# Kernel optimization log

Hardware: AMD Instinct MI355X
Metric: run time of the kernel (lower is better)

Reference implementation:

```python
import jax, jax.numpy as jnp
import numpy as np

B, N, F_IN, HID, HEADS, LAYERS = 512, 128, 128, 64, 4, 3
NEG_SLOPE = 0.2  # DenseGATConv default


def setup_inputs() -> dict:
    key = jax.random.key(0)
    ks = jax.random.split(key, 1 + 4 * LAYERS)
    inp = {}
    inp["x"] = jax.random.normal(ks[0], (B * N, F_IN), jnp.float32)
    # uniform graph sizes: graph i owns nodes [i*N, (i+1)*N)
    inp["batch_mask"] = jnp.repeat(jnp.arange(B, dtype=jnp.int32), N)
    dims = [F_IN] + [HID * HEADS] * (LAYERS - 1)
    for l in range(LAYERS):
        d = dims[l]
        k = 4 * l
        inp[f"W{l}"] = jax.random.normal(ks[1 + k], (d, HEADS * HID), jnp.float32) / np.sqrt(d)
        inp[f"att_src{l}"] = jax.random.normal(ks[2 + k], (HEADS, HID), jnp.float32) * 0.1
        inp[f"att_dst{l}"] = jax.random.normal(ks[3 + k], (HEADS, HID), jnp.float32) * 0.1
        inp[f"b{l}"] = jnp.zeros((HEADS * HID,), jnp.float32)  # zero-init bias, as in PyG
    return inp


def _dense_gat(x, adj, W, att_src, att_dst, bias):
    # x: [B, N, F_in], adj: [N, N] (shared structure, broadcast over batch)
    b, n, _ = x.shape
    h = (x @ W).reshape(b, n, HEADS, HID)                       # [B,N,H,C]
    a_src = jnp.einsum('bnhc,hc->bnh', h, att_src)              # [B,N,H]
    a_dst = jnp.einsum('bnhc,hc->bnh', h, att_dst)              # [B,N,H]
    # alpha[b,i,j,h] = a_src[b,j,h] + a_dst[b,i,h]
    alpha = a_src[:, None, :, :] + a_dst[:, :, None, :]         # [B,N,N,H]
    alpha = jnp.where(alpha >= 0, alpha, NEG_SLOPE * alpha)
    alpha = jnp.where(adj[None, :, :, None] == 0, -jnp.inf, alpha)
    alpha = jax.nn.softmax(alpha, axis=2)                       # softmax over sources j
    out = jnp.einsum('bijh,bjhc->bihc', alpha, h)               # [B,N,H,C]
    return out.reshape(b, n, HEADS * HID) + bias                # concat heads + bias


def reference(x, batch_mask, W0, att_src0, att_dst0, b0,
              W1, att_src1, att_dst1, b1, W2, att_src2, att_dst2, b2):
    # to_dense_batch with uniform graph sizes == reshape; batch_mask encodes this layout
    h = x.reshape(B, N, F_IN)
    eye = jnp.eye(N, dtype=x.dtype)
    # GNNBlock builds full adjacency with zeroed diagonal ...
    adj = jnp.ones((N, N), x.dtype) - eye
    # ... and DenseGATConv(add_loop=True) re-adds self-loops
    adj = jnp.maximum(adj, eye)
    params = [(W0, att_src0, att_dst0, b0), (W1, att_src1, att_dst1, b1),
              (W2, att_src2, att_dst2, b2)]
    for (W, a_s, a_d, b) in params:
        h = _dense_gat(h, adj, W, a_s, a_d, b)
        # block act is nn.LeakyReLU(True): negative_slope=True==1.0 -> identity
        h = jnp.where(h >= 0, h, 1.0 * h)
    return h.sum(axis=1)  # [B, HEADS*HID]
```

## Files before the change

kernel.cpp:

```cpp
#include <hip/hip_runtime.h>
#include <hip/hip_bf16.h>


typedef unsigned short u16;
typedef __attribute__((ext_vector_type(8))) short short8;
typedef __attribute__((ext_vector_type(4))) float f32x4;

#define L2E 1.44269504088896340736f

__device__ __forceinline__ u16 f2bf(float f) {
  unsigned int u = __float_as_uint(f);
  u += 0x7fffu + ((u >> 16) & 1u);
  return (u16)(u >> 16);
}
__device__ __forceinline__ unsigned int pk2(float a, float b) {
  __hip_bfloat162 h2 = __float22bfloat162_rn(make_float2(a, b));
  unsigned int u;
  __builtin_memcpy(&u, &h2, 4);
  return u;
}

__device__ __forceinline__ int xs_byte(int row, int col) {
  return (row << 9) + ((col << 1) ^ ((row & 7) << 4));
}
__device__ __forceinline__ int ht_byte(int row, int col) {
  return (row << 8) + ((col << 1) ^ ((row & 7) << 4));
}

__global__ void prep_w(const float* __restrict__ W0, const float* __restrict__ W1,
                       const float* __restrict__ W2,
                       const float* __restrict__ as0, const float* __restrict__ ad0,
                       const float* __restrict__ as1, const float* __restrict__ ad1,
                       const float* __restrict__ as2, const float* __restrict__ ad2,
                       u16* __restrict__ wt) {
  const int bid = blockIdx.x, tid = threadIdx.x;
  if (bid < 80) {
    const float* W; int NKB, base, rel;
    if (bid < 16)      { W = W0; NKB = 4; base = 0;      rel = bid; }
    else if (bid < 48) { W = W1; NKB = 8; base = 34816;  rel = bid - 16; }
    else               { W = W2; NKB = 8; base = 104448; rel = bid - 48; }
    const int kb = rel >> 2, ko = rel & 3;
    const int n = tid;
    union { u16 v[8]; short8 s; } u;
    #pragma unroll
    for (int e = 0; e < 8; ++e)
      u.v[e] = f2bf(W[(kb * 32 + ko * 8 + e) * 256 + n]);
    const int t = n >> 4, l15 = n & 15;
    *(short8*)(wt + base + (((t * NKB + kb) * 64 + l15 + (ko << 4)) << 3)) = u.s;
  } else if (bid < 100) {
    int b2 = bid - 80;
    const float* W; const float* as; const float* ad; int NKB, base, kb;
    if (b2 < 4)       { W = W0; as = as0; ad = ad0; NKB = 4; base = 0;      kb = b2; }
    else if (b2 < 12) { W = W1; as = as1; ad = ad1; NKB = 8; base = 34816;  kb = b2 - 4; }
    else              { W = W2; as = as2; ad = ad2; NKB = 8; base = 104448; kb = b2 - 12; }
    const int kloc = tid >> 3, col = tid & 7, h = col & 3;
    const int k = kb * 32 + kloc;
    const float* av = (col < 4) ? as : ad;
    float acc = 0.f;
    #pragma unroll 8
    for (int c = 0; c < 64; ++c)
      acc = fmaf(W[k * 256 + h * 64 + c], av[h * 64 + c], acc);
    const int lane2 = col + ((kloc >> 3) << 4), e = kloc & 7;
    const int tb = base + ((16 * NKB + kb) << 9);
    wt[tb + ((lane2) << 3) + e]     = f2bf(acc);
    wt[tb + ((lane2 + 8) << 3) + e] = 0;
  }
}

__global__ __launch_bounds__(1024, 4) void gat_all(
    const float* __restrict__ x, const u16* __restrict__ wt,
    const float* __restrict__ bb0, const float* __restrict__ bb1,
    const float* __restrict__ bb2, float* __restrict__ out)
{
  constexpr int AB = 0;
  constexpr int SB = 65536;
  constexpr int DB = 67584;
  constexpr int PM = 69632;
  constexpr int BS = 69696;
  constexpr int OA = 70720;
  __shared__ __align__(16) unsigned char smem[71744];

  float* sbuf  = (float*)(smem + SB);
  float* dbuf  = (float*)(smem + DB);
  float* pmaxw = (float*)(smem + PM);
  float* bsb   = (float*)(smem + BS);
  float* oac   = (float*)(smem + OA);

  const int b    = blockIdx.x;
  const int tid  = threadIdx.x;
  const int w    = tid >> 6;
  const int lane = tid & 63;
  const int l15  = lane & 15;
  const int lg   = lane >> 4;

  {
    const float4* xg = (const float4*)(x + (size_t)b * (128 * 128));
    #pragma unroll
    for (int it = 0; it < 4; ++it) {
      int e = tid + it * 1024;
      float4 v = xg[e];
      int row = e >> 5, c = (e & 31) << 2;
      uint2 u = { pk2(v.x, v.y), pk2(v.z, v.w) };
      *(uint2*)(smem + AB + xs_byte(row, c)) = u;
    }
  }
  __syncthreads();

  const u16* wfl[3]    = {wt, wt + 34816, wt + 104448};
  const float* bias[3] = {bb0, bb1, bb2};

  #pragma unroll
  for (int l = 0; l < 3; ++l) {
    const int NKB = (l == 0) ? 4 : 8;
    const u16* wf = wfl[l];

    if (tid < 256) {
      bsb[tid] = bias[l][tid];
      if (l == 2) oac[tid] = 0.f;
    }

    const int mw = w & 1, nw = w >> 1;
    f32x4 acc[4][2] = {};
    for (int ks = 0; ks < NKB; ++ks) {
      const int kcol = ks * 32 + lg * 8;
      short8 afr[4];
      #pragma unroll
      for (int mi = 0; mi < 4; ++mi)
        afr[mi] = *(const short8*)(smem + AB + xs_byte(mw * 64 + mi * 16 + l15, kcol));
      short8 bfr[2];
      #pragma unroll
      for (int ni = 0; ni < 2; ++ni) {
        int t = nw * 2 + ni;
        bfr[ni] = *(const short8*)(wf + (((t * NKB + ks) * 64 + lane) << 3));
      }
      #pragma unroll
      for (int mi = 0; mi < 4; ++mi)
        #pragma unroll
        for (int ni = 0; ni < 2; ++ni)
          acc[mi][ni] = __builtin_amdgcn_mfma_f32_16x16x32_bf16(
              afr[mi], bfr[ni], acc[mi][ni], 0, 0, 0);
    }

    if (w >= 12) {
      const int mw2 = w & 1, mih = (w >> 1) & 1;
      f32x4 acc2[2] = {};
      for (int ks = 0; ks < NKB; ++ks) {
        const int kcol = ks * 32 + lg * 8;
        short8 bsd = *(const short8*)(wf + (((16 * NKB + ks) * 64 + lane) << 3));
        #pragma unroll
        for (int mi2 = 0; mi2 < 2; ++mi2) {
          short8 a = *(const short8*)(smem + AB +
              xs_byte(mw2 * 64 + (mih * 2 + mi2) * 16 + l15, kcol));
          acc2[mi2] = __builtin_amdgcn_mfma_f32_16x16x32_bf16(a, bsd, acc2[mi2], 0, 0, 0);
        }
      }
      float mx = -3.4e38f;
      #pragma unroll
      for (int mi2 = 0; mi2 < 2; ++mi2) {
        f32x4 v = acc2[mi2] * L2E;
        if (l15 < 8) {
          float* basep = (float*)(smem + (l15 < 4 ? SB : DB))
                       + (l15 & 3) * 128 + mw2 * 64 + (mih * 2 + mi2) * 16 + lg * 4;
          *(float4*)basep = (float4){v[0], v[1], v[2], v[3]};
        }
        mx = fmaxf(mx, fmaxf(fmaxf(v[0], v[1]), fmaxf(v[2], v[3])));
      }
      mx = fmaxf(mx, __shfl_xor(mx, 16));
      mx = fmaxf(mx, __shfl_xor(mx, 32));
      if (lane < 4) pmaxw[lane * 4 + (w - 12)] = mx;
    }
    __syncthreads();

    #pragma unroll
    for (int mi = 0; mi < 4; ++mi) {
      int j0 = mw * 64 + mi * 16 + lg * 4;
      #pragma unroll
      for (int ni = 0; ni < 2; ++ni) {
        int c = nw * 32 + ni * 16 + l15;
        uint2 u = { pk2(acc[mi][ni][0], acc[mi][ni][1]),
                    pk2(acc[mi][ni][2], acc[mi][ni][3]) };
        *(uint2*)(smem + AB + ht_byte(c, j0)) = u;
      }
    }
    __syncthreads();

    {
      const int hw = w >> 2, q = w & 3;
      f32x4 facc[4][2] = {};
      float den[2] = {0.f, 0.f};
      float dvv[2], nml[2];
      const float smax = fmaxf(fmaxf(pmaxw[hw * 4], pmaxw[hw * 4 + 1]),
                               fmaxf(pmaxw[hw * 4 + 2], pmaxw[hw * 4 + 3]));
      #pragma unroll
      for (int ni = 0; ni < 2; ++ni) {
        int i = q * 32 + ni * 16 + l15;
        dvv[ni] = dbuf[hw * 128 + i];
        float tm = smax + dvv[ni];
        nml[ni] = -fmaxf(tm, 0.2f * tm);
      }
      #pragma unroll
      for (int ks = 0; ks < 4; ++ks) {
        const int j0 = ks * 32 + lg * 8;
        float4 s03 = *(const float4*)(sbuf + hw * 128 + j0);
        float4 s47 = *(const float4*)(sbuf + hw * 128 + j0 + 4);
        float sj[8] = {s03.x, s03.y, s03.z, s03.w, s47.x, s47.y, s47.z, s47.w};
        short8 afr[4];
        #pragma unroll
        for (int mi = 0; mi < 4; ++mi)
          afr[mi] = *(const short8*)(smem + AB + ht_byte(hw * 64 + mi * 16 + l15, j0));
        short8 bfr[2];
        #pragma unroll
        for (int ni = 0; ni < 2; ++ni) {
          float e[8];
          #pragma unroll
          for (int jj = 0; jj < 8; ++jj) {
            float t = sj[jj] + dvv[ni];
            t = fmaxf(t, 0.2f * t);
            e[jj] = exp2f(t + nml[ni]);
          }
          den[ni] += ((e[0] + e[1]) + (e[2] + e[3])) + ((e[4] + e[5]) + (e[6] + e[7]));
          union { short8 s; unsigned int u[4]; } pk;
          #pragma unroll
          for (int t2 = 0; t2 < 4; ++t2) pk.u[t2] = pk2(e[2 * t2], e[2 * t2 + 1]);
          bfr[ni] = pk.s;
        }
        #pragma unroll
        for (int mi = 0; mi < 4; ++mi)
          #pragma unroll
          for (int ni = 0; ni < 2; ++ni)
            facc[mi][ni] = __builtin_amdgcn_mfma_f32_16x16x32_bf16(
                afr[mi], bfr[ni], facc[mi][ni], 0, 0, 0);
      }
      float rvv[2];
      #pragma unroll
      for (int ni = 0; ni < 2; ++ni) {
        float d2 = den[ni];
        d2 += __shfl_xor(d2, 16);
        d2 += __shfl_xor(d2, 32);
        rvv[ni] = 1.f / d2;
      }
      __syncthreads();

      if (l < 2) {
        #pragma unroll
        for (int mi = 0; mi < 4; ++mi) {
          int c0 = hw * 64 + mi * 16 + lg * 4;
          float b0v = bsb[c0], b1v = bsb[c0 + 1], b2v = bsb[c0 + 2], b3v = bsb[c0 + 3];
          #pragma unroll
          for (int ni = 0; ni < 2; ++ni) {
            int i = q * 32 + ni * 16 + l15;
            float r = rvv[ni];
            uint2 u = { pk2(fmaf(facc[mi][ni][0], r, b0v), fmaf(facc[mi][ni][1], r, b1v)),
                        pk2(fmaf(facc[mi][ni][2], r, b2v), fmaf(facc[mi][ni][3], r, b3v)) };
            *(uint2*)(smem + AB + xs_byte(i, c0)) = u;
          }
        }
      } else {
        #pragma unroll
        for (int mi = 0; mi < 4; ++mi) {
          #pragma unroll
          for (int reg = 0; reg < 4; ++reg) {
            float pv2 = facc[mi][0][reg] * rvv[0] + facc[mi][1][reg] * rvv[1];
            pv2 += __shfl_xor(pv2, 1);
            pv2 += __shfl_xor(pv2, 2);
            pv2 += __shfl_xor(pv2, 4);
            pv2 += __shfl_xor(pv2, 8);
            if (l15 == 0)
              atomicAdd(&oac[hw * 64 + mi * 16 + lg * 4 + reg], pv2);
          }
        }
      }
    }
    __syncthreads();
  }

  if (tid < 256) out[(size_t)b * 256 + tid] = oac[tid] + 128.f * bsb[tid];
}

extern "C" void kernel_launch(void* const* d_in, const int* in_sizes, int n_in,
                              void* d_out, int out_size, void* d_ws, size_t ws_size,
                              hipStream_t stream) {
  const float* x   = (const float*)d_in[0];
  const float* W0  = (const float*)d_in[2];
  const float* as0 = (const float*)d_in[3];
  const float* ad0 = (const float*)d_in[4];
  const float* b0  = (const float*)d_in[5];
  const float* W1  = (const float*)d_in[6];
  const float* as1 = (const float*)d_in[7];
  const float* ad1 = (const float*)d_in[8];
  const float* b1  = (const float*)d_in[9];
  const float* W2  = (const float*)d_in[10];
  const float* as2 = (const float*)d_in[11];
  const float* ad2 = (const float*)d_in[12];
  const float* b2  = (const float*)d_in[13];
  u16* wt = (u16*)d_ws;

  hipLaunchKernelGGL(prep_w, dim3(100), dim3(256), 0, stream,
                     W0, W1, W2, as0, ad0, as1, ad1, as2, ad2, wt);
  hipLaunchKernelGGL(gat_all, dim3(512), dim3(1024), 0, stream,
                     x, wt, b0, b1, b2, (float*)d_out);
}
```

Baseline: 183.1 us.

## Halve block size to 512 threads with doubled per-wave tile work

```diff
diff --git a/kernel.cpp b/kernel.cpp
--- a/kernel.cpp
+++ b/kernel.cpp
@@ -67,7 +67,7 @@
   }
 }
 
-__global__ __launch_bounds__(1024, 4) void gat_all(
+__global__ __launch_bounds__(512, 4) void gat_all(
     const float* __restrict__ x, const u16* __restrict__ wt,
     const float* __restrict__ bb0, const float* __restrict__ bb1,
     const float* __restrict__ bb2, float* __restrict__ out)
@@ -96,8 +96,8 @@
   {
     const float4* xg = (const float4*)(x + (size_t)b * (128 * 128));
     #pragma unroll
-    for (int it = 0; it < 4; ++it) {
-      int e = tid + it * 1024;
+    for (int it = 0; it < 8; ++it) {
+      int e = tid + it * 512;
       float4 v = xg[e];
       int row = e >> 5, c = (e & 31) << 2;
       uint2 u = { pk2(v.x, v.y), pk2(v.z, v.w) };
@@ -120,28 +120,31 @@
     }
 
     const int mw = w & 1, nw = w >> 1;
-    f32x4 acc[4][2] = {};
+    f32x4 acc[4][4] = {};
     for (int ks = 0; ks < NKB; ++ks) {
       const int kcol = ks * 32 + lg * 8;
       short8 afr[4];
       #pragma unroll
       for (int mi = 0; mi < 4; ++mi)
         afr[mi] = *(const short8*)(smem + AB + xs_byte(mw * 64 + mi * 16 + l15, kcol));
-      short8 bfr[2];
-      #pragma unroll
-      for (int ni = 0; ni < 2; ++ni) {
-        int t = nw * 2 + ni;
-        bfr[ni] = *(const short8*)(wf + (((t * NKB + ks) * 64 + lane) << 3));
-      }
-      #pragma unroll
-      for (int mi = 0; mi < 4; ++mi)
-        #pragma unroll
-        for (int ni = 0; ni < 2; ++ni)
-          acc[mi][ni] = __builtin_amdgcn_mfma_f32_16x16x32_bf16(
-              afr[mi], bfr[ni], acc[mi][ni], 0, 0, 0);
-    }
-
-    if (w >= 12) {
+      #pragma unroll
+      for (int nh = 0; nh < 2; ++nh) {
+        short8 bfr[2];
+        #pragma unroll
+        for (int ni2 = 0; ni2 < 2; ++ni2) {
+          int t = nw * 4 + nh * 2 + ni2;
+          bfr[ni2] = *(const short8*)(wf + (((t * NKB + ks) * 64 + lane) << 3));
+        }
+        #pragma unroll
+        for (int mi = 0; mi < 4; ++mi)
+          #pragma unroll
+          for (int ni2 = 0; ni2 < 2; ++ni2)
+            acc[mi][nh * 2 + ni2] = __builtin_amdgcn_mfma_f32_16x16x32_bf16(
+                afr[mi], bfr[ni2], acc[mi][nh * 2 + ni2], 0, 0, 0);
+      }
+    }
+
+    if (w >= 4) {
       const int mw2 = w & 1, mih = (w >> 1) & 1;
       f32x4 acc2[2] = {};
       for (int ks = 0; ks < NKB; ++ks) {
@@ -167,7 +170,7 @@
       }
       mx = fmaxf(mx, __shfl_xor(mx, 16));
       mx = fmaxf(mx, __shfl_xor(mx, 32));
-      if (lane < 4) pmaxw[lane * 4 + (w - 12)] = mx;
+      if (lane < 4) pmaxw[lane * 4 + (w - 4)] = mx;
     }
     __syncthreads();
 
@@ -175,8 +178,8 @@
     for (int mi = 0; mi < 4; ++mi) {
       int j0 = mw * 64 + mi * 16 + lg * 4;
       #pragma unroll
-      for (int ni = 0; ni < 2; ++ni) {
-        int c = nw * 32 + ni * 16 + l15;
+      for (int ni = 0; ni < 4; ++ni) {
+        int c = nw * 64 + ni * 16 + l15;
         uint2 u = { pk2(acc[mi][ni][0], acc[mi][ni][1]),
                     pk2(acc[mi][ni][2], acc[mi][ni][3]) };
         *(uint2*)(smem + AB + ht_byte(c, j0)) = u;
@@ -185,15 +188,15 @@
     __syncthreads();
 
     {
-      const int hw = w >> 2, q = w & 3;
-      f32x4 facc[4][2] = {};
-      float den[2] = {0.f, 0.f};
-      float dvv[2], nml[2];
+      const int hw = w >> 1, ih = w & 1;
+      f32x4 facc[4][4] = {};
+      float den[4] = {0.f, 0.f, 0.f, 0.f};
+      float dvv[4], nml[4];
       const float smax = fmaxf(fmaxf(pmaxw[hw * 4], pmaxw[hw * 4 + 1]),
                                fmaxf(pmaxw[hw * 4 + 2], pmaxw[hw * 4 + 3]));
       #pragma unroll
-      for (int ni = 0; ni < 2; ++ni) {
-        int i = q * 32 + ni * 16 + l15;
+      for (int ni = 0; ni < 4; ++ni) {
+        int i = ih * 64 + ni * 16 + l15;
         dvv[ni] = dbuf[hw * 128 + i];
         float tm = smax + dvv[ni];
         nml[ni] = -fmaxf(tm, 0.2f * tm);
@@ -208,32 +211,31 @@
         #pragma unroll
         for (int mi = 0; mi < 4; ++mi)
           afr[mi] = *(const short8*)(smem + AB + ht_byte(hw * 64 + mi * 16 + l15, j0));
-        short8 bfr[2];
-        #pragma unroll
-        for (int ni = 0; ni < 2; ++ni) {
-          float e[8];
-          #pragma unroll
-          for (int jj = 0; jj < 8; ++jj) {
-            float t = sj[jj] + dvv[ni];
-            t = fmaxf(t, 0.2f * t);
-            e[jj] = exp2f(t + nml[ni]);
+        #pragma unroll
+        for (int ni = 0; ni < 4; ++ni) {
+          union { short8 s; unsigned int u[4]; } pk;
+          float dsum = 0.f;
+          #pragma unroll
+          for (int t2 = 0; t2 < 4; ++t2) {
+            float ta = sj[2 * t2] + dvv[ni];
+            ta = fmaxf(ta, 0.2f * ta);
+            float ea = exp2f(ta + nml[ni]);
+            float tb = sj[2 * t2 + 1] + dvv[ni];
+            tb = fmaxf(tb, 0.2f * tb);
+            float eb = exp2f(tb + nml[ni]);
+            dsum += ea + eb;
+            pk.u[t2] = pk2(ea, eb);
           }
-          den[ni] += ((e[0] + e[1]) + (e[2] + e[3])) + ((e[4] + e[5]) + (e[6] + e[7]));
-          union { short8 s; unsigned int u[4]; } pk;
-          #pragma unroll
-          for (int t2 = 0; t2 < 4; ++t2) pk.u[t2] = pk2(e[2 * t2], e[2 * t2 + 1]);
-          bfr[ni] = pk.s;
-        }
-        #pragma unroll
-        for (int mi = 0; mi < 4; ++mi)
-          #pragma unroll
-          for (int ni = 0; ni < 2; ++ni)
+          den[ni] += dsum;
+          #pragma unroll
+          for (int mi = 0; mi < 4; ++mi)
             facc[mi][ni] = __builtin_amdgcn_mfma_f32_16x16x32_bf16(
-                afr[mi], bfr[ni], facc[mi][ni], 0, 0, 0);
-      }
-      float rvv[2];
-      #pragma unroll
-      for (int ni = 0; ni < 2; ++ni) {
+                afr[mi], pk.s, facc[mi][ni], 0, 0, 0);
+        }
+      }
+      float rvv[4];
+      #pragma unroll
+      for (int ni = 0; ni < 4; ++ni) {
         float d2 = den[ni];
         d2 += __shfl_xor(d2, 16);
         d2 += __shfl_xor(d2, 32);
@@ -247,8 +249,8 @@
           int c0 = hw * 64 + mi * 16 + lg * 4;
           float b0v = bsb[c0], b1v = bsb[c0 + 1], b2v = bsb[c0 + 2], b3v = bsb[c0 + 3];
           #pragma unroll
-          for (int ni = 0; ni < 2; ++ni) {
-            int i = q * 32 + ni * 16 + l15;
+          for (int ni = 0; ni < 4; ++ni) {
+            int i = ih * 64 + ni * 16 + l15;
             float r = rvv[ni];
             uint2 u = { pk2(fmaf(facc[mi][ni][0], r, b0v), fmaf(facc[mi][ni][1], r, b1v)),
                         pk2(fmaf(facc[mi][ni][2], r, b2v), fmaf(facc[mi][ni][3], r, b3v)) };
@@ -260,7 +262,8 @@
         for (int mi = 0; mi < 4; ++mi) {
           #pragma unroll
           for (int reg = 0; reg < 4; ++reg) {
-            float pv2 = facc[mi][0][reg] * rvv[0] + facc[mi][1][reg] * rvv[1];
+            float pv2 = facc[mi][0][reg] * rvv[0] + facc[mi][1][reg] * rvv[1]
+                      + facc[mi][2][reg] * rvv[2] + facc[mi][3][reg] * rvv[3];
             pv2 += __shfl_xor(pv2, 1);
             pv2 += __shfl_xor(pv2, 2);
             pv2 += __shfl_xor(pv2, 4);
@@ -297,6 +300,6 @@
 
   hipLaunchKernelGGL(prep_w, dim3(100), dim3(256), 0, stream,
                      W0, W1, W2, as0, ad0, as1, ad1, as2, ad2, wt);
-  hipLaunchKernelGGL(gat_all, dim3(512), dim3(1024), 0, stream,
+  hipLaunchKernelGGL(gat_all, dim3(512), dim3(512), 0, stream,
                      x, wt, b0, b1, b2, (float*)d_out);
 }
```

Result: no change. 186.5 us (+1.9%).
